# Performance work log

Hardware: AMD Instinct MI355X
Metric: run time of the kernel (lower is better)

## Reference

```python
import jax, jax.numpy as jnp
import numpy as np

TOP_K = 8


def setup_inputs() -> dict:
    key = jax.random.key(0)
    k1, k2 = jax.random.split(key)
    hidden_states = jax.random.normal(k1, (4, 4096, 4096), dtype=jnp.float32)
    weight = jax.random.normal(k2, (64, 4096), dtype=jnp.float32) * 0.02
    return {"hidden_states": hidden_states, "weight": weight}


def reference(hidden_states, weight):
    # Flatten [B, S, H] -> [T, H]; gating math is done in float32 (matches .float()).
    h = hidden_states.shape[-1]
    x = hidden_states.reshape(-1, h).astype(jnp.float32)
    # Router logits: [T, E] = [T, H] @ [H, E]
    logits = jnp.einsum('th,eh->te', x, weight.astype(jnp.float32))
    scores = jax.nn.softmax(logits, axis=-1)
    # Top-k expert selection (greedy router)
    topk_weight, topk_idx = jax.lax.top_k(scores, TOP_K)  # [T, K], [T, K]
    # Normalize top-k probabilities (norm_topk_prob=True)
    denom = jnp.sum(topk_weight, axis=-1, keepdims=True) + 1e-20
    topk_weight = topk_weight / denom
    return topk_weight, topk_idx
```

## Files before the change

kernel.cpp:

```cpp
#include <hip/hip_runtime.h>
#include <math.h>

typedef float  f32x4  __attribute__((ext_vector_type(4)));
typedef int    i32x4  __attribute__((ext_vector_type(4)));

#define H      4096
#define E      64
#define TOPK   8
#define TILE_T 16
#define CK     256
#define MS     4
#define NCH    16

__global__ __launch_bounds__(256)
void prep_w(const float* __restrict__ Wg, signed char* __restrict__ Wb)
{
  int n = blockIdx.x * 256 + threadIdx.x;
  int kgrp = n & 3, m = (n >> 2) & 63, e = n >> 8;
  const float* wp = Wg + e * 4096 + m * 64 + kgrp * 16;
  signed char lb[5][16];
  #pragma unroll
  for (int s = 0; s < 16; ++s) {
    long long v = (long long)rint((double)wp[s] * 2199023255552.0);
    #pragma unroll
    for (int j = 0; j < 4; ++j) {
      signed char b = (signed char)(v & 0xff);
      lb[j][s] = b;
      v = (v - b) >> 8;
    }
    lb[4][s] = (signed char)v;
  }
  int lanei = (kgrp << 4) | (e & 15);
  int eq = e >> 4;
  #pragma unroll
  for (int j = 0; j < 5; ++j) {
    i32x4 d;
    #pragma unroll
    for (int r = 0; r < 4; ++r)
      d[r] = (lb[j][4*r] & 0xFF) | ((lb[j][4*r+1] & 0xFF) << 8)
           | ((lb[j][4*r+2] & 0xFF) << 16) | ((lb[j][4*r+3] & 0xFF) << 24);
    *(i32x4*)(Wb + (((size_t)(m * 4 + eq) * 5 + j) << 10) + lanei * 16) = d;
  }
}

__global__ __launch_bounds__(64)
void comp_w(const float* __restrict__ Wg, double* __restrict__ compT)
{
  int e = blockIdx.x;
  int lane = threadIdx.x;
  double s = 0.0;
  #pragma unroll 4
  for (int i = 0; i < 64; ++i)
    s += rint((double)Wg[e * 4096 + i * 64 + lane] * 2199023255552.0);
  #pragma unroll
  for (int off = 32; off >= 1; off >>= 1)
    s += __shfl_xor(s, off);
  if (lane == 0) compT[e] = 8421504.0 * s;
}

__global__ __launch_bounds__(256)
void moe_gate_i8(const float* __restrict__ X, const signed char* __restrict__ Wb,
                 const double* __restrict__ compT, float* __restrict__ out,
                 int n_tokens)
{
  __shared__ char As[16384];
  double* Ls = (double*)As;

  const int tid  = threadIdx.x;
  const int lane = tid & 63;
  const int w    = tid >> 6;
  const int t0   = blockIdx.x * TILE_T;
  const int l15  = lane & 15;
  const int kg   = lane >> 4;

  i32x4 z = {0, 0, 0, 0};
  int lab = l15 * 0x01010101;
  i32x4 onev = {0x01010101, 0x01010101, 0x01010101, 0x01010101};
  i32x4 labv = {lab, lab, lab, lab};
  i32x4 pr = __builtin_amdgcn_mfma_i32_16x16x64_i8(labv, onev, z, 0, 0, 0);
  i32x4 pc = __builtin_amdgcn_mfma_i32_16x16x64_i8(onev, labv, z, 0, 0, 0);
  int qrow[4], qcol[4];
  #pragma unroll
  for (int r = 0; r < 4; ++r) { qrow[r] = pr[r] >> 6; qcol[r] = pc[r] >> 6; }

  i32x4 acc3 = z, acc4 = z, acc5 = z, acc6 = z, acc7 = z;

  const int kgrp = lane >> 2;
  const int wrd  = lane & 3;
  const int swzs = ((lane >> 3) & 7) << 4;
  const float* xbase = X + (size_t)t0 * H + lane * 4;

  const signed char* bpp = Wb + w * 5120 + lane * 16;

  for (int c = 0; c < NCH; ++c) {
    f32x4 xr[4];
    #pragma unroll
    for (int q = 0; q < 4; ++q)
      xr[q] = *(const f32x4*)(xbase + (size_t)(w * 4 + q) * H + c * CK);

    #pragma unroll
    for (int q = 0; q < 4; ++q) {
      const int r = w * 4 + q;
      unsigned u0 = ((unsigned)(int)(xr[q][0] * 268435456.0f)) ^ 0x00808080u;
      unsigned u1 = ((unsigned)(int)(xr[q][1] * 268435456.0f)) ^ 0x00808080u;
      unsigned u2 = ((unsigned)(int)(xr[q][2] * 268435456.0f)) ^ 0x00808080u;
      unsigned u3 = ((unsigned)(int)(xr[q][3] * 268435456.0f)) ^ 0x00808080u;
      unsigned p01, p23, W0, W1, W2, W3;
      p01 = __builtin_amdgcn_perm(u1, u0, 0x04000400u);
      p23 = __builtin_amdgcn_perm(u3, u2, 0x04000400u);
      W0  = __builtin_amdgcn_perm(p23, p01, 0x05040100u);
      p01 = __builtin_amdgcn_perm(u1, u0, 0x05010501u);
      p23 = __builtin_amdgcn_perm(u3, u2, 0x05010501u);
      W1  = __builtin_amdgcn_perm(p23, p01, 0x05040100u);
      p01 = __builtin_amdgcn_perm(u1, u0, 0x06020602u);
      p23 = __builtin_amdgcn_perm(u3, u2, 0x06020602u);
      W2  = __builtin_amdgcn_perm(p23, p01, 0x05040100u);
      p01 = __builtin_amdgcn_perm(u1, u0, 0x07030703u);
      p23 = __builtin_amdgcn_perm(u3, u2, 0x07030703u);
      W3  = __builtin_amdgcn_perm(p23, p01, 0x05040100u);
      char* base = As + (kgrp << 10) + (((r << 4) ^ swzs)) + (wrd << 2);
      *(unsigned*)(base + 0x000) = W0;
      *(unsigned*)(base + 0x100) = W1;
      *(unsigned*)(base + 0x200) = W2;
      *(unsigned*)(base + 0x300) = W3;
    }
    __syncthreads();

    #pragma unroll
    for (int m = 0; m < MS; ++m) {
      const int kq   = 4 * m + kg;
      const int swzr = ((kq >> 1) & 7) << 4;
      const char* abase = As + (kq << 10) + (((l15 << 4) ^ swzr));
      i32x4 a0 = *(const i32x4*)(abase + 0x000);
      i32x4 a1 = *(const i32x4*)(abase + 0x100);
      i32x4 a2 = *(const i32x4*)(abase + 0x200);
      i32x4 a3 = *(const i32x4*)(abase + 0x300);
      i32x4 b0 = *(const i32x4*)(bpp);
      i32x4 b1 = *(const i32x4*)(bpp + 1024);
      i32x4 b2 = *(const i32x4*)(bpp + 2048);
      i32x4 b3 = *(const i32x4*)(bpp + 3072);
      i32x4 b4 = *(const i32x4*)(bpp + 4096);
      bpp += 20480;
      acc3 = __builtin_amdgcn_mfma_i32_16x16x64_i8(a0, b3, acc3, 0, 0, 0);
      acc4 = __builtin_amdgcn_mfma_i32_16x16x64_i8(a0, b4, acc4, 0, 0, 0);
      acc5 = __builtin_amdgcn_mfma_i32_16x16x64_i8(a1, b4, acc5, 0, 0, 0);
      acc6 = __builtin_amdgcn_mfma_i32_16x16x64_i8(a2, b4, acc6, 0, 0, 0);
      acc7 = __builtin_amdgcn_mfma_i32_16x16x64_i8(a3, b4, acc7, 0, 0, 0);
      acc3 = __builtin_amdgcn_mfma_i32_16x16x64_i8(a1, b2, acc3, 0, 0, 0);
      acc4 = __builtin_amdgcn_mfma_i32_16x16x64_i8(a1, b3, acc4, 0, 0, 0);
      acc5 = __builtin_amdgcn_mfma_i32_16x16x64_i8(a2, b3, acc5, 0, 0, 0);
      acc6 = __builtin_amdgcn_mfma_i32_16x16x64_i8(a3, b3, acc6, 0, 0, 0);
      acc3 = __builtin_amdgcn_mfma_i32_16x16x64_i8(a2, b1, acc3, 0, 0, 0);
      acc4 = __builtin_amdgcn_mfma_i32_16x16x64_i8(a2, b2, acc4, 0, 0, 0);
      acc5 = __builtin_amdgcn_mfma_i32_16x16x64_i8(a3, b2, acc5, 0, 0, 0);
      acc3 = __builtin_amdgcn_mfma_i32_16x16x64_i8(a3, b0, acc3, 0, 0, 0);
      acc4 = __builtin_amdgcn_mfma_i32_16x16x64_i8(a3, b1, acc4, 0, 0, 0);
    }
    __syncthreads();
  }

  #pragma unroll
  for (int r = 0; r < 4; ++r) {
    int ex = w * 16 + qcol[r];
    double part = (16777216.0              * (double)acc3[r]
                 + 4294967296.0            * (double)acc4[r]
                 + 1099511627776.0         * (double)acc5[r]
                 + 281474976710656.0       * (double)acc6[r]
                 + 72057594037927936.0     * (double)acc7[r]
                 + compT[ex]) * 1.6940658945086007e-21;
    Ls[qrow[r] * E + ex] = part;
  }
  __syncthreads();

  for (int tt2 = 0; tt2 < 4; tt2++) {
    int t = w * 4 + tt2;
    double val = Ls[t * E + lane];

    double mx = val;
    #pragma unroll
    for (int off = 32; off >= 1; off >>= 1)
      mx = fmax(mx, __shfl_xor(mx, off));

    float p = expf((float)(val - mx));
    float S = p;
    #pragma unroll
    for (int off = 32; off >= 1; off >>= 1)
      S += __shfl_xor(S, off);

    double cur = val;
    float myw = 0.f; int myidx = 0;
    float psum = 0.f;
    #pragma unroll
    for (int r = 0; r < TOPK; r++) {
      double v = cur; int ii = lane;
      #pragma unroll
      for (int off = 32; off >= 1; off >>= 1) {
        double ov = __shfl_xor(v, off);
        int    oi = __shfl_xor(ii, off);
        if (ov > v || (ov == v && oi < ii)) { v = ov; ii = oi; }
      }
      float pw = __shfl(p, ii);
      psum += pw;
      if (lane == r) { myw = pw; myidx = ii; }
      if (lane == ii) cur = -INFINITY;
    }
    float denom = psum + 1e-20f * S;
    if (lane < TOPK) {
      size_t gt = (size_t)(t0 + t);
      out[gt * TOPK + lane] = myw / denom;
      out[(size_t)n_tokens * TOPK + gt * TOPK + lane] = (float)myidx;
    }
  }
}

extern "C" void kernel_launch(void* const* d_in, const int* in_sizes, int n_in,
                              void* d_out, int out_size, void* d_ws, size_t ws_size,
                              hipStream_t stream)
{
  const float* X  = (const float*)d_in[0];
  const float* Wg = (const float*)d_in[1];
  float* out = (float*)d_out;
  signed char* Wb = (signed char*)d_ws;
  double* compT   = (double*)((char*)d_ws + 1310720);
  int n_tokens = in_sizes[0] / H;

  prep_w<<<64, 256, 0, stream>>>(Wg, Wb);
  comp_w<<<64, 64, 0, stream>>>(Wg, compT);
  moe_gate_i8<<<n_tokens / TILE_T, 256, 0, stream>>>(X, Wb, compT, out, n_tokens);
}
```

Before: 118.8 us.

## Double-buffer LDS activation tile and prefetch next chunk during MFMA

```diff
diff --git a/kernel.cpp b/kernel.cpp
--- a/kernel.cpp
+++ b/kernel.cpp
@@ -63,7 +63,7 @@
                  const double* __restrict__ compT, float* __restrict__ out,
                  int n_tokens)
 {
-  __shared__ char As[16384];
+  __shared__ char As[32768];
   double* Ls = (double*)As;
 
   const int tid  = threadIdx.x;
@@ -92,72 +92,96 @@
 
   const signed char* bpp = Wb + w * 5120 + lane * 16;
 
+  f32x4 xr[4];
+
+  #define CONVWRITE(boff_)                                                    \
+  {                                                                           \
+    _Pragma("unroll")                                                         \
+    for (int q = 0; q < 4; ++q) {                                             \
+      const int r = w * 4 + q;                                                \
+      unsigned u0 = ((unsigned)(int)(xr[q][0] * 268435456.0f)) ^ 0x00808080u; \
+      unsigned u1 = ((unsigned)(int)(xr[q][1] * 268435456.0f)) ^ 0x00808080u; \
+      unsigned u2 = ((unsigned)(int)(xr[q][2] * 268435456.0f)) ^ 0x00808080u; \
+      unsigned u3 = ((unsigned)(int)(xr[q][3] * 268435456.0f)) ^ 0x00808080u; \
+      unsigned p01, p23, W0, W1, W2, W3;                                      \
+      p01 = __builtin_amdgcn_perm(u1, u0, 0x04000400u);                       \
+      p23 = __builtin_amdgcn_perm(u3, u2, 0x04000400u);                       \
+      W0  = __builtin_amdgcn_perm(p23, p01, 0x05040100u);                     \
+      p01 = __builtin_amdgcn_perm(u1, u0, 0x05010501u);                       \
+      p23 = __builtin_amdgcn_perm(u3, u2, 0x05010501u);                       \
+      W1  = __builtin_amdgcn_perm(p23, p01, 0x05040100u);                     \
+      p01 = __builtin_amdgcn_perm(u1, u0, 0x06020602u);                       \
+      p23 = __builtin_amdgcn_perm(u3, u2, 0x06020602u);                       \
+      W2  = __builtin_amdgcn_perm(p23, p01, 0x05040100u);                     \
+      p01 = __builtin_amdgcn_perm(u1, u0, 0x07030703u);                       \
+      p23 = __builtin_amdgcn_perm(u3, u2, 0x07030703u);                       \
+      W3  = __builtin_amdgcn_perm(p23, p01, 0x05040100u);                     \
+      char* base = As + (boff_) + (kgrp << 10) + (((r << 4) ^ swzs))          \
+                 + (wrd << 2);                                                \
+      *(unsigned*)(base + 0x000) = W0;                                        \
+      *(unsigned*)(base + 0x100) = W1;                                        \
+      *(unsigned*)(base + 0x200) = W2;                                        \
+      *(unsigned*)(base + 0x300) = W3;                                        \
+    }                                                                         \
+  }
+
+  #pragma unroll
+  for (int q = 0; q < 4; ++q)
+    xr[q] = *(const f32x4*)(xbase + (size_t)(w * 4 + q) * H);
+  CONVWRITE(0);
+  __syncthreads();
+
   for (int c = 0; c < NCH; ++c) {
-    f32x4 xr[4];
-    #pragma unroll
-    for (int q = 0; q < 4; ++q)
-      xr[q] = *(const f32x4*)(xbase + (size_t)(w * 4 + q) * H + c * CK);
-
-    #pragma unroll
-    for (int q = 0; q < 4; ++q) {
-      const int r = w * 4 + q;
-      unsigned u0 = ((unsigned)(int)(xr[q][0] * 268435456.0f)) ^ 0x00808080u;
-      unsigned u1 = ((unsigned)(int)(xr[q][1] * 268435456.0f)) ^ 0x00808080u;
-      unsigned u2 = ((unsigned)(int)(xr[q][2] * 268435456.0f)) ^ 0x00808080u;
-      unsigned u3 = ((unsigned)(int)(xr[q][3] * 268435456.0f)) ^ 0x00808080u;
-      unsigned p01, p23, W0, W1, W2, W3;
-      p01 = __builtin_amdgcn_perm(u1, u0, 0x04000400u);
-      p23 = __builtin_amdgcn_perm(u3, u2, 0x04000400u);
-      W0  = __builtin_amdgcn_perm(p23, p01, 0x05040100u);
-      p01 = __builtin_amdgcn_perm(u1, u0, 0x05010501u);
-      p23 = __builtin_amdgcn_perm(u3, u2, 0x05010501u);
-      W1  = __builtin_amdgcn_perm(p23, p01, 0x05040100u);
-      p01 = __builtin_amdgcn_perm(u1, u0, 0x06020602u);
-      p23 = __builtin_amdgcn_perm(u3, u2, 0x06020602u);
-      W2  = __builtin_amdgcn_perm(p23, p01, 0x05040100u);
-      p01 = __builtin_amdgcn_perm(u1, u0, 0x07030703u);
-      p23 = __builtin_amdgcn_perm(u3, u2, 0x07030703u);
-      W3  = __builtin_amdgcn_perm(p23, p01, 0x05040100u);
-      char* base = As + (kgrp << 10) + (((r << 4) ^ swzs)) + (wrd << 2);
-      *(unsigned*)(base + 0x000) = W0;
-      *(unsigned*)(base + 0x100) = W1;
-      *(unsigned*)(base + 0x200) = W2;
-      *(unsigned*)(base + 0x300) = W3;
-    }
+    i32x4 bf[4][5];
+    #pragma unroll
+    for (int m = 0; m < MS; ++m)
+      #pragma unroll
+      for (int j = 0; j < 5; ++j)
+        bf[m][j] = *(const i32x4*)(bpp + (size_t)m * 20480 + (j << 10));
+    bpp += (size_t)MS * 20480;
+    __builtin_amdgcn_sched_barrier(0);
+
+    if (c < NCH - 1) {
+      #pragma unroll
+      for (int q = 0; q < 4; ++q)
+        xr[q] = *(const f32x4*)(xbase + (size_t)(w * 4 + q) * H + (c + 1) * CK);
+    }
+    __builtin_amdgcn_sched_barrier(0);
+
+    {
+      const char* base_ = As + ((c & 1) << 14);
+      #pragma unroll
+      for (int m = 0; m < MS; ++m) {
+        const int kq   = 4 * m + kg;
+        const int swzr = ((kq >> 1) & 7) << 4;
+        const char* abase = base_ + (kq << 10) + (((l15 << 4) ^ swzr));
+        i32x4 a0 = *(const i32x4*)(abase + 0x000);
+        i32x4 a1 = *(const i32x4*)(abase + 0x100);
+        i32x4 a2 = *(const i32x4*)(abase + 0x200);
+        i32x4 a3 = *(const i32x4*)(abase + 0x300);
+        i32x4 b0 = bf[m][0], b1 = bf[m][1], b2 = bf[m][2];
+        i32x4 b3 = bf[m][3], b4 = bf[m][4];
+        acc3 = __builtin_amdgcn_mfma_i32_16x16x64_i8(a0, b3, acc3, 0, 0, 0);
+        acc4 = __builtin_amdgcn_mfma_i32_16x16x64_i8(a0, b4, acc4, 0, 0, 0);
+        acc5 = __builtin_amdgcn_mfma_i32_16x16x64_i8(a1, b4, acc5, 0, 0, 0);
+        acc6 = __builtin_amdgcn_mfma_i32_16x16x64_i8(a2, b4, acc6, 0, 0, 0);
+        acc7 = __builtin_amdgcn_mfma_i32_16x16x64_i8(a3, b4, acc7, 0, 0, 0);
+        acc3 = __builtin_amdgcn_mfma_i32_16x16x64_i8(a1, b2, acc3, 0, 0, 0);
+        acc4 = __builtin_amdgcn_mfma_i32_16x16x64_i8(a1, b3, acc4, 0, 0, 0);
+        acc5 = __builtin_amdgcn_mfma_i32_16x16x64_i8(a2, b3, acc5, 0, 0, 0);
+        acc6 = __builtin_amdgcn_mfma_i32_16x16x64_i8(a3, b3, acc6, 0, 0, 0);
+        acc3 = __builtin_amdgcn_mfma_i32_16x16x64_i8(a2, b1, acc3, 0, 0, 0);
+        acc4 = __builtin_amdgcn_mfma_i32_16x16x64_i8(a2, b2, acc4, 0, 0, 0);
+        acc5 = __builtin_amdgcn_mfma_i32_16x16x64_i8(a3, b2, acc5, 0, 0, 0);
+        acc3 = __builtin_amdgcn_mfma_i32_16x16x64_i8(a3, b0, acc3, 0, 0, 0);
+        acc4 = __builtin_amdgcn_mfma_i32_16x16x64_i8(a3, b1, acc4, 0, 0, 0);
+      }
+    }
+
+    if (c < NCH - 1) CONVWRITE(((c + 1) & 1) << 14);
     __syncthreads();
-
-    #pragma unroll
-    for (int m = 0; m < MS; ++m) {
-      const int kq   = 4 * m + kg;
-      const int swzr = ((kq >> 1) & 7) << 4;
-      const char* abase = As + (kq << 10) + (((l15 << 4) ^ swzr));
-      i32x4 a0 = *(const i32x4*)(abase + 0x000);
-      i32x4 a1 = *(const i32x4*)(abase + 0x100);
-      i32x4 a2 = *(const i32x4*)(abase + 0x200);
-      i32x4 a3 = *(const i32x4*)(abase + 0x300);
-      i32x4 b0 = *(const i32x4*)(bpp);
-      i32x4 b1 = *(const i32x4*)(bpp + 1024);
-      i32x4 b2 = *(const i32x4*)(bpp + 2048);
-      i32x4 b3 = *(const i32x4*)(bpp + 3072);
-      i32x4 b4 = *(const i32x4*)(bpp + 4096);
-      bpp += 20480;
-      acc3 = __builtin_amdgcn_mfma_i32_16x16x64_i8(a0, b3, acc3, 0, 0, 0);
-      acc4 = __builtin_amdgcn_mfma_i32_16x16x64_i8(a0, b4, acc4, 0, 0, 0);
-      acc5 = __builtin_amdgcn_mfma_i32_16x16x64_i8(a1, b4, acc5, 0, 0, 0);
-      acc6 = __builtin_amdgcn_mfma_i32_16x16x64_i8(a2, b4, acc6, 0, 0, 0);
-      acc7 = __builtin_amdgcn_mfma_i32_16x16x64_i8(a3, b4, acc7, 0, 0, 0);
-      acc3 = __builtin_amdgcn_mfma_i32_16x16x64_i8(a1, b2, acc3, 0, 0, 0);
-      acc4 = __builtin_amdgcn_mfma_i32_16x16x64_i8(a1, b3, acc4, 0, 0, 0);
-      acc5 = __builtin_amdgcn_mfma_i32_16x16x64_i8(a2, b3, acc5, 0, 0, 0);
-      acc6 = __builtin_amdgcn_mfma_i32_16x16x64_i8(a3, b3, acc6, 0, 0, 0);
-      acc3 = __builtin_amdgcn_mfma_i32_16x16x64_i8(a2, b1, acc3, 0, 0, 0);
-      acc4 = __builtin_amdgcn_mfma_i32_16x16x64_i8(a2, b2, acc4, 0, 0, 0);
-      acc5 = __builtin_amdgcn_mfma_i32_16x16x64_i8(a3, b2, acc5, 0, 0, 0);
-      acc3 = __builtin_amdgcn_mfma_i32_16x16x64_i8(a3, b0, acc3, 0, 0, 0);
-      acc4 = __builtin_amdgcn_mfma_i32_16x16x64_i8(a3, b1, acc4, 0, 0, 0);
-    }
-    __syncthreads();
-  }
+  }
+  #undef CONVWRITE
 
   #pragma unroll
   for (int r = 0; r < 4; ++r) {
```

New measurement: 124.7 us. 4.9% more time.

## Split the K dimension across two blocks with atomic accumulation and a separate finalize kernel

Applied to the files above, without the earlier changes.

```diff
diff --git a/kernel.cpp b/kernel.cpp
--- a/kernel.cpp
+++ b/kernel.cpp
@@ -3,6 +3,7 @@
 
 typedef float  f32x4  __attribute__((ext_vector_type(4)));
 typedef int    i32x4  __attribute__((ext_vector_type(4)));
+typedef double f64x4  __attribute__((ext_vector_type(4)));
 
 #define H      4096
 #define E      64
@@ -10,7 +11,11 @@
 #define TILE_T 16
 #define CK     256
 #define MS     4
-#define NCH    16
+#define NCH    8
+
+#define WB_OFF   0
+#define COMP_OFF 1310720
+#define LG_OFF   2097152
 
 __global__ __launch_bounds__(256)
 void prep_w(const float* __restrict__ Wg, signed char* __restrict__ Wb)
@@ -46,30 +51,41 @@
 __global__ __launch_bounds__(64)
 void comp_w(const float* __restrict__ Wg, double* __restrict__ compT)
 {
-  int e = blockIdx.x;
+  int b = blockIdx.x;
+  int kH = b >> 6, e = b & 63;
   int lane = threadIdx.x;
   double s = 0.0;
   #pragma unroll 4
-  for (int i = 0; i < 64; ++i)
-    s += rint((double)Wg[e * 4096 + i * 64 + lane] * 2199023255552.0);
+  for (int i = 0; i < 32; ++i)
+    s += rint((double)Wg[e * 4096 + kH * 2048 + i * 64 + lane] * 2199023255552.0);
   #pragma unroll
   for (int off = 32; off >= 1; off >>= 1)
     s += __shfl_xor(s, off);
-  if (lane == 0) compT[e] = 8421504.0 * s;
-}
-
-__global__ __launch_bounds__(256)
-void moe_gate_i8(const float* __restrict__ X, const signed char* __restrict__ Wb,
-                 const double* __restrict__ compT, float* __restrict__ out,
-                 int n_tokens)
+  if (lane == 0) compT[kH * 64 + e] = 8421504.0 * s;
+}
+
+__global__ __launch_bounds__(256)
+void zero_lg(double* __restrict__ lg)
+{
+  size_t i = ((size_t)blockIdx.x * 256 + threadIdx.x) * 4;
+  f64x4 z4 = {0.0, 0.0, 0.0, 0.0};
+  *(f64x4*)(lg + i) = z4;
+}
+
+__global__ __launch_bounds__(256)
+void moe_part(const float* __restrict__ X, const signed char* __restrict__ Wb,
+              const double* __restrict__ compT, double* __restrict__ lg)
 {
   __shared__ char As[16384];
-  double* Ls = (double*)As;
+
+  const int bid  = blockIdx.x;
+  const int tile = bid >> 1;
+  const int kH   = bid & 1;
+  const int t0   = tile * TILE_T;
 
   const int tid  = threadIdx.x;
   const int lane = tid & 63;
   const int w    = tid >> 6;
-  const int t0   = blockIdx.x * TILE_T;
   const int l15  = lane & 15;
   const int kg   = lane >> 4;
 
@@ -88,9 +104,9 @@
   const int kgrp = lane >> 2;
   const int wrd  = lane & 3;
   const int swzs = ((lane >> 3) & 7) << 4;
-  const float* xbase = X + (size_t)t0 * H + lane * 4;
-
-  const signed char* bpp = Wb + w * 5120 + lane * 16;
+  const float* xbase = X + (size_t)t0 * H + kH * 2048 + lane * 4;
+
+  const signed char* bpp = Wb + (size_t)(kH * 128 + w) * 5120 + lane * 16;
 
   for (int c = 0; c < NCH; ++c) {
     f32x4 xr[4];
@@ -167,14 +183,22 @@
                  + 1099511627776.0         * (double)acc5[r]
                  + 281474976710656.0       * (double)acc6[r]
                  + 72057594037927936.0     * (double)acc7[r]
-                 + compT[ex]) * 1.6940658945086007e-21;
-    Ls[qrow[r] * E + ex] = part;
-  }
-  __syncthreads();
-
-  for (int tt2 = 0; tt2 < 4; tt2++) {
-    int t = w * 4 + tt2;
-    double val = Ls[t * E + lane];
+                 + compT[kH * 64 + ex]) * 1.6940658945086007e-21;
+    unsafeAtomicAdd(&lg[(size_t)(t0 + qrow[r]) * E + ex], part);
+  }
+}
+
+__global__ __launch_bounds__(256)
+void moe_fin(const double* __restrict__ lg, float* __restrict__ out,
+             int n_tokens)
+{
+  const int tid  = threadIdx.x;
+  const int lane = tid & 63;
+  const int wv   = tid >> 6;
+
+  for (int i = 0; i < 16; ++i) {
+    int t = blockIdx.x * 64 + wv * 16 + i;
+    double val = lg[(size_t)t * E + lane];
 
     double mx = val;
     #pragma unroll
@@ -206,7 +230,7 @@
     }
     float denom = psum + 1e-20f * S;
     if (lane < TOPK) {
-      size_t gt = (size_t)(t0 + t);
+      size_t gt = (size_t)t;
       out[gt * TOPK + lane] = myw / denom;
       out[(size_t)n_tokens * TOPK + gt * TOPK + lane] = (float)myidx;
     }
@@ -220,11 +244,14 @@
   const float* X  = (const float*)d_in[0];
   const float* Wg = (const float*)d_in[1];
   float* out = (float*)d_out;
-  signed char* Wb = (signed char*)d_ws;
-  double* compT   = (double*)((char*)d_ws + 1310720);
+  signed char* Wb = (signed char*)((char*)d_ws + WB_OFF);
+  double* compT   = (double*)((char*)d_ws + COMP_OFF);
+  double* lg      = (double*)((char*)d_ws + LG_OFF);
   int n_tokens = in_sizes[0] / H;
 
   prep_w<<<64, 256, 0, stream>>>(Wg, Wb);
-  comp_w<<<64, 64, 0, stream>>>(Wg, compT);
-  moe_gate_i8<<<n_tokens / TILE_T, 256, 0, stream>>>(X, Wb, compT, out, n_tokens);
-}
+  comp_w<<<128, 64, 0, stream>>>(Wg, compT);
+  zero_lg<<<1024, 256, 0, stream>>>(lg);
+  moe_part<<<(n_tokens / TILE_T) * 2, 256, 0, stream>>>(X, Wb, compT, lg);
+  moe_fin<<<n_tokens / 64, 256, 0, stream>>>(lg, out, n_tokens);
+}
```

Result: slower. 184.3 us (+55.1%).
